# Kernel tuning notes

Measured on AMD Instinct MI355X. Metric: run time of the kernel, lower is better.

## Reference

```python
import jax, jax.numpy as jnp
import numpy as np

LN_EPS = 1e-5


def setup_inputs() -> dict:
    key = jax.random.key(0)
    k1, = jax.random.split(key, 1)
    B, C, H, W = 16, 512, 64, 64
    HW = H * W
    x = jax.random.normal(k1, (B, C, H, W), dtype=jnp.float32)
    gamma = jnp.ones((), dtype=jnp.float32)          # Scale(1) learnable scalar
    ln_weight = jnp.ones((HW,), dtype=jnp.float32)   # LayerNorm weight
    ln_bias = jnp.zeros((HW,), dtype=jnp.float32)    # LayerNorm bias
    return {"x": x, "gamma": gamma, "ln_weight": ln_weight, "ln_bias": ln_bias}


def reference(x, gamma, ln_weight, ln_bias):
    B, C, H, W = x.shape
    v = x.reshape(B, C, H * W)                       # [B, C, HW] (Q = K = V)
    energy = jnp.einsum('bcn,bdn->bcd', v, v)        # [B, C, C]
    attn = jax.nn.softmax(energy, axis=-1)
    out = jnp.einsum('bcd,bdn->bcn', attn, v)        # [B, C, HW]
    out = gamma * out + v                            # scale + residual
    # LayerNorm over last dim (HW), torch eps=1e-5
    mean = jnp.mean(out, axis=-1, keepdims=True)
    var = jnp.mean(jnp.square(out - mean), axis=-1, keepdims=True)
    out = (out - mean) * jax.lax.rsqrt(var + LN_EPS) * ln_weight + ln_bias
    return out.reshape(B, C, H, W)
```

## Files before the change

### kernel.cpp

```cpp
#include <hip/hip_runtime.h>
#include <hip/hip_bf16.h>

#define B_DIM 16
#define C_DIM 512
#define HW_DIM 4096
#define LN_EPS 1e-5f

using bf16 = __hip_bfloat16;
typedef __bf16 v8bf __attribute__((ext_vector_type(8)));
typedef float v4f __attribute__((ext_vector_type(4)));
typedef unsigned short v8us __attribute__((ext_vector_type(8)));
typedef unsigned short v4us __attribute__((ext_vector_type(4)));
using gptr_t = const __attribute__((address_space(1))) void*;
using lptr_t = __attribute__((address_space(3))) void*;

__device__ __forceinline__ unsigned short f2bf(float f) {
  unsigned int u = __float_as_uint(f);
  u = (u + 0x7fffu + ((u >> 16) & 1u)) >> 16;
  return (unsigned short)u;
}
__device__ __forceinline__ float bf2f(unsigned short us) {
  return __uint_as_float(((unsigned int)us) << 16);
}

__global__ __launch_bounds__(256) void k_convert_transpose(
    const float* __restrict__ x, unsigned short* __restrict__ v,
    unsigned short* __restrict__ vt) {
  __shared__ unsigned short tile[64 * 64];
  const int tid = threadIdx.x;
  const int b = blockIdx.z;
  const int n0 = blockIdx.x * 64;
  const int c0 = blockIdx.y * 64;
  const size_t boff = (size_t)b * ((size_t)C_DIM * HW_DIM);
  const float* xb = x + boff;
  unsigned short* vb = v + boff;
  unsigned short* vtb = vt + boff;

  const int cl = tid >> 3;
  const int hb = tid & 7;
  const int h8 = hb * 8;
#pragma unroll
  for (int j = 0; j < 2; ++j) {
    const int c = cl + j * 32;
    const float* src = xb + (size_t)(c0 + c) * HW_DIM + n0 + h8;
    const float4 f0 = ((const float4*)src)[0];
    const float4 f1 = ((const float4*)src)[1];
    v8us pack;
    pack[0] = f2bf(f0.x); pack[1] = f2bf(f0.y);
    pack[2] = f2bf(f0.z); pack[3] = f2bf(f0.w);
    pack[4] = f2bf(f1.x); pack[5] = f2bf(f1.y);
    pack[6] = f2bf(f1.z); pack[7] = f2bf(f1.w);
    *(v8us*)(vb + (size_t)(c0 + c) * HW_DIM + n0 + h8) = pack;
    const int key = (c & 7) ^ ((c >> 3) & 7);
    *(v8us*)(tile + c * 64 + ((hb ^ key) << 3)) = pack;
  }
  __syncthreads();
  const int nl = tid >> 3;
  const int c8 = (tid & 7) * 8;
  const int n = 2 * nl;
  v8us pa, pb;
#pragma unroll
  for (int e = 0; e < 8; ++e) {
    const int r = c8 + e;
    const int key = (r & 7) ^ ((r >> 3) & 7);
    const unsigned int w = *(const unsigned int*)(
        tile + r * 64 + (((n >> 3) ^ key) << 3) + (n & 7));
    pa[e] = (unsigned short)(w & 0xffffu);
    pb[e] = (unsigned short)(w >> 16);
  }
  *(v8us*)(vtb + (size_t)(n0 + n) * C_DIM + c0 + c8) = pa;
  *(v8us*)(vtb + (size_t)(n0 + n + 1) * C_DIM + c0 + c8) = pb;
}

#define TILE_E (256 * 64)

__device__ __forceinline__ void stage_half8s(
    const bf16* __restrict__ g, bf16* l, int k0, int stride, int wave, int lane) {
  const int lrow = lane >> 3, lc = lane & 7;
#pragma unroll
  for (int i = 0; i < 2; ++i) {
    const int row = i * 64 + wave * 8 + lrow;
    __builtin_amdgcn_global_load_lds(
        (gptr_t)(g + (size_t)row * stride + k0 + ((lc ^ (row & 7)) << 3)),
        (lptr_t)(l + (i * 64 + wave * 8) * 64), 16, 0, 0);
  }
}
__device__ __forceinline__ void stage_op2s(
    const bf16* __restrict__ g, bf16* l, int k0, int stride, int wave, int lane) {
  stage_half8s(g, l, k0, stride, wave, lane);
  stage_half8s(g + (size_t)128 * stride, l + 128 * 64, k0, stride, wave, lane);
}
__device__ __forceinline__ void stage_half8(
    const bf16* __restrict__ g, bf16* l, int k0, int wave, int lane) {
  const int lrow = lane >> 3, lc = lane & 7;
#pragma unroll
  for (int i = 0; i < 2; ++i) {
    const int row = i * 64 + wave * 8 + lrow;
    __builtin_amdgcn_global_load_lds(
        (gptr_t)(g + (size_t)row * C_DIM + k0 + ((lc ^ (row & 7)) << 3)),
        (lptr_t)(l + (i * 64 + wave * 8) * 64), 16, 0, 0);
  }
}
__device__ __forceinline__ void stage_op2(
    const bf16* __restrict__ g, bf16* l, int k0, int wave, int lane) {
  stage_half8(g, l, k0, wave, lane);
  stage_half8(g + (size_t)128 * C_DIM, l + 128 * 64, k0, wave, lane);
}
__device__ __forceinline__ v8bf ld_frag8(const bf16* l, int row, int j) {
  return *(const v8bf*)(l + row * 64 + ((j ^ (row & 7)) << 3));
}

__device__ __forceinline__ void gemm_8ph_loop(
    const bf16* __restrict__ Ab, const bf16* __restrict__ Bb,
    const int strideA, const int strideB, const int kts,
    bf16* smem, const int wave, const int lane, v4f acc[8][4]) {
  const int wm = wave >> 2, wn = wave & 3;
  const int rl = lane & 15, kq = lane >> 4;

  stage_op2s(Bb, smem + 2 * TILE_E, 0, strideB, wave, lane);
  stage_op2s(Ab, smem, 0, strideA, wave, lane);
  stage_op2s(Bb, smem + 3 * TILE_E, 64, strideB, wave, lane);
  stage_op2s(Ab, smem + TILE_E, 64, strideA, wave, lane);
  asm volatile("s_waitcnt vmcnt(8)" ::: "memory");
  __builtin_amdgcn_s_barrier();

  v8bf a[4][2], b01[2][2], b23[2][2];
  for (int kt = 0; kt < kts; ++kt) {
    const bf16* LA = smem + (kt & 1) * TILE_E;
    const bf16* LB = smem + (2 + (kt & 1)) * TILE_E;
    bf16* SA = smem + (kt & 1) * TILE_E;
    bf16* SB = smem + (2 + (kt & 1)) * TILE_E;
#pragma unroll
    for (int mi = 0; mi < 4; ++mi)
#pragma unroll
      for (int kk = 0; kk < 2; ++kk)
        a[mi][kk] = ld_frag8(LA, wm * 128 + mi * 16 + rl, kk * 4 + kq);
#pragma unroll
    for (int ni = 0; ni < 2; ++ni)
#pragma unroll
      for (int kk = 0; kk < 2; ++kk)
        b01[ni][kk] = ld_frag8(LB, wn * 64 + ni * 16 + rl, kk * 4 + kq);
    __builtin_amdgcn_s_barrier();
    asm volatile("s_waitcnt lgkmcnt(0)");
    __builtin_amdgcn_s_setprio(1);
#pragma unroll
    for (int kk = 0; kk < 2; ++kk)
#pragma unroll
      for (int mi = 0; mi < 4; ++mi)
#pragma unroll
        for (int ni = 0; ni < 2; ++ni)
          acc[mi][ni] = __builtin_amdgcn_mfma_f32_16x16x32_bf16(
              a[mi][kk], b01[ni][kk], acc[mi][ni], 0, 0, 0);
    __builtin_amdgcn_s_setprio(0);
    __builtin_amdgcn_s_barrier();
#pragma unroll
    for (int ni = 0; ni < 2; ++ni)
#pragma unroll
      for (int kk = 0; kk < 2; ++kk)
        b23[ni][kk] = ld_frag8(LB, wn * 64 + (ni + 2) * 16 + rl, kk * 4 + kq);
    __builtin_amdgcn_s_barrier();
    asm volatile("s_waitcnt lgkmcnt(0)");
    __builtin_amdgcn_s_setprio(1);
#pragma unroll
    for (int kk = 0; kk < 2; ++kk)
#pragma unroll
      for (int mi = 0; mi < 4; ++mi)
#pragma unroll
        for (int ni = 0; ni < 2; ++ni)
          acc[mi][ni + 2] = __builtin_amdgcn_mfma_f32_16x16x32_bf16(
              a[mi][kk], b23[ni][kk], acc[mi][ni + 2], 0, 0, 0);
    __builtin_amdgcn_s_setprio(0);
    __builtin_amdgcn_s_barrier();
#pragma unroll
    for (int mi = 0; mi < 4; ++mi)
#pragma unroll
      for (int kk = 0; kk < 2; ++kk)
        a[mi][kk] = ld_frag8(LA, wm * 128 + (mi + 4) * 16 + rl, kk * 4 + kq);
    if (kt < kts - 2) stage_op2s(Bb, SB, (kt + 2) * 64, strideB, wave, lane);
    __builtin_amdgcn_s_barrier();
    asm volatile("s_waitcnt lgkmcnt(0)");
    __builtin_amdgcn_s_setprio(1);
#pragma unroll
    for (int kk = 0; kk < 2; ++kk)
#pragma unroll
      for (int mi = 0; mi < 4; ++mi)
#pragma unroll
        for (int ni = 0; ni < 2; ++ni)
          acc[mi + 4][ni + 2] = __builtin_amdgcn_mfma_f32_16x16x32_bf16(
              a[mi][kk], b23[ni][kk], acc[mi + 4][ni + 2], 0, 0, 0);
    __builtin_amdgcn_s_setprio(0);
    __builtin_amdgcn_s_barrier();
    if (kt < kts - 2) stage_op2s(Ab, SA, (kt + 2) * 64, strideA, wave, lane);
    __builtin_amdgcn_s_barrier();
    __builtin_amdgcn_s_setprio(1);
#pragma unroll
    for (int kk = 0; kk < 2; ++kk)
#pragma unroll
      for (int mi = 0; mi < 4; ++mi)
#pragma unroll
        for (int ni = 0; ni < 2; ++ni)
          acc[mi + 4][ni] = __builtin_amdgcn_mfma_f32_16x16x32_bf16(
              a[mi][kk], b01[ni][kk], acc[mi + 4][ni], 0, 0, 0);
    __builtin_amdgcn_s_setprio(0);
    if (kt < kts - 2)
      asm volatile("s_waitcnt vmcnt(8)" ::: "memory");
    else if (kt == kts - 2)
      asm volatile("s_waitcnt vmcnt(0)" ::: "memory");
    __builtin_amdgcn_s_barrier();
  }
}

__device__ __forceinline__ void epilogue_bounce(
    v4f acc[8][4], bf16* smem, float* ob, const int out_stride,
    const int wave, const int lane) {
  const int wm = wave >> 2, wn = wave & 3;
  const int rl = lane & 15, kq = lane >> 4;
  float* smf = (float*)smem;
#pragma unroll
  for (int h = 0; h < 2; ++h) {
    if (wm == h) {
#pragma unroll
      for (int mi = 0; mi < 8; ++mi)
#pragma unroll
        for (int ni = 0; ni < 4; ++ni)
#pragma unroll
          for (int rr = 0; rr < 4; ++rr) {
            const int rloc = mi * 16 + kq * 4 + rr;
            const int col = wn * 64 + ni * 16 + rl;
            const int key = rloc & 7;
            smf[rloc * 256 + ((((col >> 2) ^ key) << 2) | (col & 3))] =
                acc[mi][ni][rr];
          }
    }
    __syncthreads();
#pragma unroll
    for (int it = 0; it < 16; ++it) {
      const int rloc = it * 8 + wave;
      const float4 vv =
          *(const float4*)(smf + rloc * 256 + ((lane ^ (rloc & 7)) << 2));
      *(float4*)(ob + (size_t)(h * 128 + rloc) * out_stride + lane * 4) = vv;
    }
    __syncthreads();
  }
}

__global__ __launch_bounds__(512, 2) void k_gemm1(
    const bf16* __restrict__ v, float* __restrict__ e_part) {
  __shared__ __align__(16) bf16 smem[4 * TILE_E];
  const int bid = blockIdx.x;
  const int t = (bid & 7) * 32 + (bid >> 3);
  const int ks = t & 3;
  const int db = (t >> 2) & 1;
  const int cb = (t >> 3) & 1;
  const int b = t >> 4;
  const int tid = threadIdx.x;
  const int wave = tid >> 6, lane = tid & 63;

  const bf16* vb = v + (size_t)b * ((size_t)C_DIM * HW_DIM) + ks * 1024;
  const bf16* Ab = vb + (size_t)(cb * 256) * HW_DIM;
  const bf16* Bb = vb + (size_t)(db * 256) * HW_DIM;

  v4f acc[8][4] = {};
  gemm_8ph_loop(Ab, Bb, HW_DIM, HW_DIM, 16, smem, wave, lane, acc);

  float* ob = e_part + (size_t)ks * ((size_t)B_DIM * C_DIM * C_DIM) +
              (size_t)b * (C_DIM * C_DIM) + (size_t)(cb * 256) * C_DIM + db * 256;
  epilogue_bounce(acc, smem, ob, C_DIM, wave, lane);
}

__global__ __launch_bounds__(256) void k_softmax(
    const float* __restrict__ e_part, unsigned short* __restrict__ attn) {
  const int row = blockIdx.x;
  const size_t bcc = (size_t)B_DIM * C_DIM * C_DIM;
  const float* e0 = e_part + (size_t)row * C_DIM;
  const int tid = threadIdx.x;
  float v0 = 0.f, v1 = 0.f;
#pragma unroll
  for (int p = 0; p < 4; ++p) {
    v0 += e0[p * bcc + tid];
    v1 += e0[p * bcc + tid + 256];
  }
  float mx = fmaxf(v0, v1);
#pragma unroll
  for (int off = 32; off > 0; off >>= 1) mx = fmaxf(mx, __shfl_xor(mx, off));
  __shared__ float rmax[4], rsum[4];
  const int wv = tid >> 6, ln = tid & 63;
  if (ln == 0) rmax[wv] = mx;
  __syncthreads();
  mx = fmaxf(fmaxf(rmax[0], rmax[1]), fmaxf(rmax[2], rmax[3]));
  const float p0 = __expf(v0 - mx), p1 = __expf(v1 - mx);
  float s = p0 + p1;
#pragma unroll
  for (int off = 32; off > 0; off >>= 1) s += __shfl_xor(s, off);
  if (ln == 0) rsum[wv] = s;
  __syncthreads();
  s = rsum[0] + rsum[1] + rsum[2] + rsum[3];
  const float inv = 1.0f / s;
  attn[(size_t)row * C_DIM + tid] = f2bf(p0 * inv);
  attn[(size_t)row * C_DIM + tid + 256] = f2bf(p1 * inv);
}

__global__ __launch_bounds__(512, 2) void k_gemm2(
    const bf16* __restrict__ attn, const bf16* __restrict__ vt,
    unsigned short* __restrict__ av) {
  __shared__ __align__(16) bf16 smem[4 * TILE_E];
  const int bid = blockIdx.x;
  const int t = (bid & 7) * 64 + (bid >> 3);
  const int b = t >> 5;
  const int cb = (t >> 4) & 1;
  const int nb = t & 15;
  const int tid = threadIdx.x;
  const int wave = tid >> 6, lane = tid & 63;
  const int wm = wave >> 2, wn = wave & 3;
  const int rl = lane & 15, kq = lane >> 4;

  const bf16* Ab = attn + (size_t)b * (C_DIM * C_DIM) + (size_t)(cb * 256) * C_DIM;
  const bf16* Bb = vt + (size_t)b * ((size_t)C_DIM * HW_DIM) + (size_t)(nb * 256) * C_DIM;

  v4f acc[8][4] = {};

  stage_op2(Bb, smem + 2 * TILE_E, 0, wave, lane);
  stage_op2(Ab, smem, 0, wave, lane);
  stage_op2(Bb, smem + 3 * TILE_E, 64, wave, lane);
  stage_op2(Ab, smem + TILE_E, 64, wave, lane);
  asm volatile("s_waitcnt vmcnt(8)" ::: "memory");
  __builtin_amdgcn_s_barrier();

  v8bf a[4][2], b01[2][2], b23[2][2];
  for (int kt = 0; kt < 8; ++kt) {
    const bf16* LA = smem + (kt & 1) * TILE_E;
    const bf16* LB = smem + (2 + (kt & 1)) * TILE_E;
    bf16* SA = smem + (kt & 1) * TILE_E;
    bf16* SB = smem + (2 + (kt & 1)) * TILE_E;
#pragma unroll
    for (int mi = 0; mi < 4; ++mi)
#pragma unroll
      for (int kk = 0; kk < 2; ++kk)
        a[mi][kk] = ld_frag8(LA, wm * 128 + mi * 16 + rl, kk * 4 + kq);
#pragma unroll
    for (int ni = 0; ni < 2; ++ni)
#pragma unroll
      for (int kk = 0; kk < 2; ++kk)
        b01[ni][kk] = ld_frag8(LB, wn * 64 + ni * 16 + rl, kk * 4 + kq);
    __builtin_amdgcn_s_barrier();
    asm volatile("s_waitcnt lgkmcnt(0)");
    __builtin_amdgcn_s_setprio(1);
#pragma unroll
    for (int kk = 0; kk < 2; ++kk)
#pragma unroll
      for (int mi = 0; mi < 4; ++mi)
#pragma unroll
        for (int ni = 0; ni < 2; ++ni)
          acc[mi][ni] = __builtin_amdgcn_mfma_f32_16x16x32_bf16(
              a[mi][kk], b01[ni][kk], acc[mi][ni], 0, 0, 0);
    __builtin_amdgcn_s_setprio(0);
    __builtin_amdgcn_s_barrier();
#pragma unroll
    for (int ni = 0; ni < 2; ++ni)
#pragma unroll
      for (int kk = 0; kk < 2; ++kk)
        b23[ni][kk] = ld_frag8(LB, wn * 64 + (ni + 2) * 16 + rl, kk * 4 + kq);
    __builtin_amdgcn_s_barrier();
    asm volatile("s_waitcnt lgkmcnt(0)");
    __builtin_amdgcn_s_setprio(1);
#pragma unroll
    for (int kk = 0; kk < 2; ++kk)
#pragma unroll
      for (int mi = 0; mi < 4; ++mi)
#pragma unroll
        for (int ni = 0; ni < 2; ++ni)
          acc[mi][ni + 2] = __builtin_amdgcn_mfma_f32_16x16x32_bf16(
              a[mi][kk], b23[ni][kk], acc[mi][ni + 2], 0, 0, 0);
    __builtin_amdgcn_s_setprio(0);
    __builtin_amdgcn_s_barrier();
#pragma unroll
    for (int mi = 0; mi < 4; ++mi)
#pragma unroll
      for (int kk = 0; kk < 2; ++kk)
        a[mi][kk] = ld_frag8(LA, wm * 128 + (mi + 4) * 16 + rl, kk * 4 + kq);
    if (kt < 6) stage_op2(Bb, SB, (kt + 2) * 64, wave, lane);
    __builtin_amdgcn_s_barrier();
    asm volatile("s_waitcnt lgkmcnt(0)");
    __builtin_amdgcn_s_setprio(1);
#pragma unroll
    for (int kk = 0; kk < 2; ++kk)
#pragma unroll
      for (int mi = 0; mi < 4; ++mi)
#pragma unroll
        for (int ni = 0; ni < 2; ++ni)
          acc[mi + 4][ni + 2] = __builtin_amdgcn_mfma_f32_16x16x32_bf16(
              a[mi][kk], b23[ni][kk], acc[mi + 4][ni + 2], 0, 0, 0);
    __builtin_amdgcn_s_setprio(0);
    __builtin_amdgcn_s_barrier();
    if (kt < 6) stage_op2(Ab, SA, (kt + 2) * 64, wave, lane);
    __builtin_amdgcn_s_barrier();
    __builtin_amdgcn_s_setprio(1);
#pragma unroll
    for (int kk = 0; kk < 2; ++kk)
#pragma unroll
      for (int mi = 0; mi < 4; ++mi)
#pragma unroll
        for (int ni = 0; ni < 2; ++ni)
          acc[mi + 4][ni] = __builtin_amdgcn_mfma_f32_16x16x32_bf16(
              a[mi][kk], b01[ni][kk], acc[mi + 4][ni], 0, 0, 0);
    __builtin_amdgcn_s_setprio(0);
    if (kt < 6)
      asm volatile("s_waitcnt vmcnt(8)" ::: "memory");
    else if (kt == 6)
      asm volatile("s_waitcnt vmcnt(0)" ::: "memory");
    __builtin_amdgcn_s_barrier();
  }

  float* smf = (float*)smem;
  unsigned short* ob = av + (size_t)b * ((size_t)C_DIM * HW_DIM) +
                       (size_t)(cb * 256) * HW_DIM + nb * 256;
#pragma unroll
  for (int h = 0; h < 2; ++h) {
    if (wm == h) {
#pragma unroll
      for (int mi = 0; mi < 8; ++mi)
#pragma unroll
        for (int ni = 0; ni < 4; ++ni)
#pragma unroll
          for (int rr = 0; rr < 4; ++rr) {
            const int rloc = mi * 16 + kq * 4 + rr;
            const int col = wn * 64 + ni * 16 + rl;
            const int key = rloc & 7;
            smf[rloc * 256 + ((((col >> 2) ^ key) << 2) | (col & 3))] =
                acc[mi][ni][rr];
          }
    }
    __syncthreads();
#pragma unroll
    for (int it = 0; it < 16; ++it) {
      const int rloc = it * 8 + wave;
      const float4 vv =
          *(const float4*)(smf + rloc * 256 + ((lane ^ (rloc & 7)) << 2));
      v4us p;
      p[0] = f2bf(vv.x); p[1] = f2bf(vv.y);
      p[2] = f2bf(vv.z); p[3] = f2bf(vv.w);
      *(v4us*)(ob + (size_t)(h * 128 + rloc) * HW_DIM + lane * 4) = p;
    }
    __syncthreads();
  }
}

__global__ __launch_bounds__(256) void k_ln(
    float* __restrict__ out, const unsigned short* __restrict__ av,
    const unsigned short* __restrict__ vres,
    const float* __restrict__ gamma, const float* __restrict__ w,
    const float* __restrict__ bias) {
  const int row = blockIdx.x;
  float* p = out + (size_t)row * HW_DIM;
  const unsigned short* ap = av + (size_t)row * HW_DIM;
  const unsigned short* vr = vres + (size_t)row * HW_DIM;
  const float g = gamma[0];
  const int tid = threadIdx.x;
  float4 vals[4];
  float s = 0.f, ss = 0.f;
#pragma unroll
  for (int i = 0; i < 4; ++i) {
    const int idx = tid + i * 256;
    const v4us au = *(const v4us*)(ap + idx * 4);
    const v4us rv = *(const v4us*)(vr + idx * 4);
    float4 vv;
    vv.x = g * bf2f(au[0]) + bf2f(rv[0]);
    vv.y = g * bf2f(au[1]) + bf2f(rv[1]);
    vv.z = g * bf2f(au[2]) + bf2f(rv[2]);
    vv.w = g * bf2f(au[3]) + bf2f(rv[3]);
    vals[i] = vv;
    s += vv.x + vv.y + vv.z + vv.w;
    ss += vv.x * vv.x + vv.y * vv.y + vv.z * vv.z + vv.w * vv.w;
  }
#pragma unroll
  for (int off = 32; off > 0; off >>= 1) {
    s += __shfl_xor(s, off);
    ss += __shfl_xor(ss, off);
  }
  __shared__ float rs[4], rss[4];
  const int wv = tid >> 6, ln = tid & 63;
  if (ln == 0) { rs[wv] = s; rss[wv] = ss; }
  __syncthreads();
  s = rs[0] + rs[1] + rs[2] + rs[3];
  ss = rss[0] + rss[1] + rss[2] + rss[3];
  const float mean = s * (1.f / HW_DIM);
  const float var = ss * (1.f / HW_DIM) - mean * mean;
  const float rstd = rsqrtf(var + LN_EPS);
#pragma unroll
  for (int i = 0; i < 4; ++i) {
    const int idx = tid + i * 256;
    const float4 vv = vals[i];
    const float4 w4 = ((const float4*)w)[idx];
    const float4 b4 = ((const float4*)bias)[idx];
    float4 r;
    r.x = (vv.x - mean) * rstd * w4.x + b4.x;
    r.y = (vv.y - mean) * rstd * w4.y + b4.y;
    r.z = (vv.z - mean) * rstd * w4.z + b4.z;
    r.w = (vv.w - mean) * rstd * w4.w + b4.w;
    ((float4*)p)[idx] = r;
  }
}

extern "C" void kernel_launch(void* const* d_in, const int* in_sizes, int n_in,
                              void* d_out, int out_size, void* d_ws, size_t ws_size,
                              hipStream_t stream) {
  const float* x = (const float*)d_in[0];
  const float* gamma = (const float*)d_in[1];
  const float* lnw = (const float*)d_in[2];
  const float* lnb = (const float*)d_in[3];
  float* out = (float*)d_out;
  char* ws = (char*)d_ws;

  const size_t n_elem = (size_t)B_DIM * C_DIM * HW_DIM;
  const size_t e_elems = (size_t)B_DIM * C_DIM * C_DIM;
  unsigned short* vbf = (unsigned short*)ws;
  unsigned short* vbfT = (unsigned short*)(ws + 2 * n_elem);
  float* e_part = (float*)(ws + 4 * n_elem);
  unsigned short* attn =
      (unsigned short*)(ws + 4 * n_elem + 4 * e_elems * sizeof(float));
  unsigned short* av = (unsigned short*)(ws + 4 * n_elem +
                                         4 * e_elems * sizeof(float) +
                                         2 * e_elems);

  k_convert_transpose<<<dim3(HW_DIM / 64, C_DIM / 64, B_DIM), 256, 0, stream>>>(
      x, vbf, vbfT);
  k_gemm1<<<256, 512, 0, stream>>>((const bf16*)vbf, e_part);
  k_softmax<<<B_DIM * C_DIM, 256, 0, stream>>>(e_part, attn);
  k_gemm2<<<512, 512, 0, stream>>>((const bf16*)attn, (const bf16*)vbfT, av);
  k_ln<<<B_DIM * C_DIM, 256, 0, stream>>>(out, av, vbf, gamma, lnw, lnb);
}
```

Before: 212.9 us.

## Split fused bf16 convert-transpose into separate convert and transpose kernels

```diff
diff --git a/kernel.cpp b/kernel.cpp
--- a/kernel.cpp
+++ b/kernel.cpp
@@ -23,53 +23,50 @@
   return __uint_as_float(((unsigned int)us) << 16);
 }
 
-__global__ __launch_bounds__(256) void k_convert_transpose(
-    const float* __restrict__ x, unsigned short* __restrict__ v,
-    unsigned short* __restrict__ vt) {
-  __shared__ unsigned short tile[64 * 64];
-  const int tid = threadIdx.x;
-  const int b = blockIdx.z;
-  const int n0 = blockIdx.x * 64;
-  const int c0 = blockIdx.y * 64;
-  const size_t boff = (size_t)b * ((size_t)C_DIM * HW_DIM);
-  const float* xb = x + boff;
-  unsigned short* vb = v + boff;
-  unsigned short* vtb = vt + boff;
-
-  const int cl = tid >> 3;
-  const int hb = tid & 7;
-  const int h8 = hb * 8;
-#pragma unroll
-  for (int j = 0; j < 2; ++j) {
-    const int c = cl + j * 32;
-    const float* src = xb + (size_t)(c0 + c) * HW_DIM + n0 + h8;
-    const float4 f0 = ((const float4*)src)[0];
-    const float4 f1 = ((const float4*)src)[1];
+__global__ __launch_bounds__(256) void k_convert(
+    const float* __restrict__ x, unsigned short* __restrict__ v) {
+  const size_t i0 = ((size_t)blockIdx.x * 256 + threadIdx.x) * 8;
+  const size_t step = (size_t)2048 * 256 * 8;
+#pragma unroll
+  for (int it = 0; it < 8; ++it) {
+    const size_t base = i0 + (size_t)it * step;
+    const float4 f0 = ((const float4*)(x + base))[0];
+    const float4 f1 = ((const float4*)(x + base))[1];
     v8us pack;
     pack[0] = f2bf(f0.x); pack[1] = f2bf(f0.y);
     pack[2] = f2bf(f0.z); pack[3] = f2bf(f0.w);
     pack[4] = f2bf(f1.x); pack[5] = f2bf(f1.y);
     pack[6] = f2bf(f1.z); pack[7] = f2bf(f1.w);
-    *(v8us*)(vb + (size_t)(c0 + c) * HW_DIM + n0 + h8) = pack;
-    const int key = (c & 7) ^ ((c >> 3) & 7);
-    *(v8us*)(tile + c * 64 + ((hb ^ key) << 3)) = pack;
-  }
-  __syncthreads();
-  const int nl = tid >> 3;
-  const int c8 = (tid & 7) * 8;
-  const int n = 2 * nl;
-  v8us pa, pb;
-#pragma unroll
-  for (int e = 0; e < 8; ++e) {
-    const int r = c8 + e;
-    const int key = (r & 7) ^ ((r >> 3) & 7);
-    const unsigned int w = *(const unsigned int*)(
-        tile + r * 64 + (((n >> 3) ^ key) << 3) + (n & 7));
-    pa[e] = (unsigned short)(w & 0xffffu);
-    pb[e] = (unsigned short)(w >> 16);
-  }
-  *(v8us*)(vtb + (size_t)(n0 + n) * C_DIM + c0 + c8) = pa;
-  *(v8us*)(vtb + (size_t)(n0 + n + 1) * C_DIM + c0 + c8) = pb;
+    *(v8us*)(v + base) = pack;
+  }
+}
+
+__global__ __launch_bounds__(256) void k_transpose(
+    const unsigned short* __restrict__ v, unsigned short* __restrict__ vt) {
+  __shared__ unsigned short lds[64 * 20];
+  const int tid = threadIdx.x;
+  const int b = blockIdx.z;
+  const int n0 = blockIdx.x * 16;
+  const size_t boff = (size_t)b * ((size_t)C_DIM * HW_DIM);
+  const unsigned short* vb = v + boff;
+  unsigned short* vtb = vt + boff;
+  const int cr = tid >> 2;
+  const int nq = tid & 3;
+  const int rr = tid >> 4;
+  const int kk4 = (tid & 15) * 4;
+#pragma unroll
+  for (int i = 0; i < 8; ++i) {
+    const int ci = i * 64;
+    const v4us in =
+        *(const v4us*)(vb + (size_t)(ci + cr) * HW_DIM + n0 + nq * 4);
+    *(v4us*)(lds + cr * 20 + nq * 4) = in;
+    __syncthreads();
+    v4us outp;
+#pragma unroll
+    for (int j = 0; j < 4; ++j) outp[j] = lds[(kk4 + j) * 20 + rr];
+    *(v4us*)(vtb + (size_t)(n0 + rr) * C_DIM + ci + kk4) = outp;
+    __syncthreads();
+  }
 }
 
 #define TILE_E (256 * 64)
@@ -522,8 +519,8 @@
                                          4 * e_elems * sizeof(float) +
                                          2 * e_elems);
 
-  k_convert_transpose<<<dim3(HW_DIM / 64, C_DIM / 64, B_DIM), 256, 0, stream>>>(
-      x, vbf, vbfT);
+  k_convert<<<2048, 256, 0, stream>>>(x, vbf);
+  k_transpose<<<dim3(HW_DIM / 16, 1, B_DIM), 256, 0, stream>>>(vbf, vbfT);
   k_gemm1<<<256, 512, 0, stream>>>((const bf16*)vbf, e_part);
   k_softmax<<<B_DIM * C_DIM, 256, 0, stream>>>(e_part, attn);
   k_gemm2<<<512, 512, 0, stream>>>((const bf16*)attn, (const bf16*)vbfT, av);
```

Result: slower. 244.0 us (+14.6%).
